# Optimization experiments

Measured on AMD Instinct MI355X. Metric: run time of the kernel, lower is better.

Reference implementation:

```python
import jax, jax.numpy as jnp
import numpy as np

N, IN, OUT, RANK = 8192, 4096, 4096, 16
SCALING = 2.0

def setup_inputs() -> dict:
    key = jax.random.key(0)
    k1, k2, k3, k4 = jax.random.split(key, 4)
    x = jax.random.normal(k1, (N, IN), dtype=jnp.float32)
    weight = jax.random.normal(k2, (OUT, IN), dtype=jnp.float32) * (1.0 / np.sqrt(IN))
    lora_A = jax.random.normal(k3, (RANK, IN), dtype=jnp.float32) * (1.0 / np.sqrt(IN))
    lora_B = jax.random.normal(k4, (OUT, RANK), dtype=jnp.float32) * 0.01
    return {"x": x, "weight": weight, "lora_A": lora_A, "lora_B": lora_B}

def reference(x, weight, lora_A, lora_B):
    # frozen base linear: F.linear(x, weight) == x @ weight.T  -> [N, OUT]
    base = jnp.einsum('ni,oi->no', x, weight)
    # LoRA branch: dropout(x) (p=0 => identity) @ A.T @ B.T, scaled
    lora = jnp.einsum('ni,ri->nr', x, lora_A)      # [N, RANK]
    lora = jnp.einsum('nr,or->no', lora, lora_B)   # [N, OUT]
    return base + lora * SCALING
```

## Files before the change

kernel.cpp:

```cpp
#include <hip/hip_runtime.h>


#define N_ROWS 8192
#define K_DIM  4096
#define N_COLS 4096
#define RANK   16
#define BK     64
#define NT     (K_DIM / BK)

typedef __bf16 bf16x8 __attribute__((ext_vector_type(8)));
typedef float  f32x4  __attribute__((ext_vector_type(4)));

__device__ __forceinline__ unsigned short f2bf(float f) {
  unsigned int u = __builtin_bit_cast(unsigned int, f);
  u += 0x7FFFu + ((u >> 16) & 1u);
  return (unsigned short)(u >> 16);
}


__global__ __launch_bounds__(256) void conv_x_kernel(const float* __restrict__ x,
                                                     unsigned short* __restrict__ xb) {
  size_t idx = (size_t)blockIdx.x * blockDim.x + threadIdx.x;
  const float4 v = *reinterpret_cast<const float4*>(x + idx * 4);
  ushort4 r;
  r.x = f2bf(v.x); r.y = f2bf(v.y); r.z = f2bf(v.z); r.w = f2bf(v.w);
  *reinterpret_cast<ushort4*>(xb + idx * 4) = r;
}

__global__ __launch_bounds__(256) void make_weff_kernel(const float* __restrict__ w,
                                                        const float* __restrict__ A,
                                                        const float* __restrict__ Bm,
                                                        unsigned short* __restrict__ wb) {
  size_t idx = (size_t)blockIdx.x * blockDim.x + threadIdx.x;
  int o  = (int)(idx >> 10);
  int ic = (int)(idx & 1023) << 2;
  const float4 wv = *reinterpret_cast<const float4*>(w + (size_t)o * K_DIM + ic);
  float a0 = wv.x, a1 = wv.y, a2 = wv.z, a3 = wv.w;
  float br[RANK];
#pragma unroll
  for (int r4 = 0; r4 < RANK / 4; ++r4) {
    const float4 bv = *reinterpret_cast<const float4*>(Bm + (size_t)o * RANK + r4 * 4);
    br[r4 * 4 + 0] = bv.x; br[r4 * 4 + 1] = bv.y;
    br[r4 * 4 + 2] = bv.z; br[r4 * 4 + 3] = bv.w;
  }
#pragma unroll
  for (int r = 0; r < RANK; ++r) {
    const float4 av = *reinterpret_cast<const float4*>(A + (size_t)r * K_DIM + ic);
    float b2 = br[r] * 2.0f;
    a0 += b2 * av.x; a1 += b2 * av.y; a2 += b2 * av.z; a3 += b2 * av.w;
  }
  ushort4 rr;
  rr.x = f2bf(a0); rr.y = f2bf(a1); rr.z = f2bf(a2); rr.w = f2bf(a3);
  *reinterpret_cast<ushort4*>(wb + (size_t)o * K_DIM + ic) = rr;
}


__device__ __forceinline__ void gload_lds16(const void* g, void* l) {
  __builtin_amdgcn_global_load_lds(
      (__attribute__((address_space(1))) void*)g,
      (__attribute__((address_space(3))) void*)l, 16, 0, 0);
}

__global__ __launch_bounds__(512, 2) void gemm_bf16_8phase(
    const unsigned short* __restrict__ xb, const unsigned short* __restrict__ wb,
    float* __restrict__ out) {
  __shared__ __align__(16) char smem[131072];

  const int t  = threadIdx.x;
  const int l  = t & 63;
  const int wv = t >> 6;
  const int lr = l & 15;
  const int lk = l >> 4;
  const int wr = wv >> 2;
  const int wc = wv & 3;

  const int bid  = blockIdx.x;
  const int sbid = (bid & 7) * 64 + (bid >> 3);
  const int bm   = sbid >> 4;
  const int bn   = sbid & 15;

  const int srow = t >> 3;
  const int scol = ((t & 7) ^ ((t >> 3) & 7)) << 3;
  const unsigned short* gA = xb + (size_t)(bm * 256 + srow) * K_DIM + scol;
  const unsigned short* gB = wb + (size_t)(bn * 256 + srow) * K_DIM + scol;
  char* ldsA = smem + t * 16;
  char* ldsB = smem + 65536 + t * 16;

#define STAGE_A(hh, tk, bufb) do {                                              \
    const unsigned short* _g = gA + (size_t)((hh) * 128) * K_DIM + (size_t)(tk) * BK; \
    char* _l = ldsA + (bufb) * 32768 + (hh) * 16384;                            \
    gload_lds16(_g, _l);                                                        \
    gload_lds16(_g + (size_t)64 * K_DIM, _l + 8192);                            \
  } while (0)
#define STAGE_B(hh, tk, bufb) do {                                              \
    const unsigned short* _g = gB + (size_t)((hh) * 128) * K_DIM + (size_t)(tk) * BK; \
    char* _l = ldsB + (bufb) * 32768 + (hh) * 16384;                            \
    gload_lds16(_g, _l);                                                        \
    gload_lds16(_g + (size_t)64 * K_DIM, _l + 8192);                            \
  } while (0)

  const int g0   = (lk ^ (lr & 7)) << 4;
  const int g1   = ((lk + 4) ^ (lr & 7)) << 4;
  const int aoff = (wr * 16 + lr) * 128;
  const int boff = (wc * 16 + lr) * 128;

  bf16x8 aF[8];
  bf16x8 bF[4];
  f32x4 acc[8][4];
#pragma unroll
  for (int m = 0; m < 8; ++m)
#pragma unroll
    for (int n = 0; n < 4; ++n)
      acc[m][n] = (f32x4){0.f, 0.f, 0.f, 0.f};

#define READ_A(hh, bufo) do {                                                   \
    const char* _b = smem + (bufo) + (hh) * 16384 + aoff;                       \
    aF[0] = *(const bf16x8*)(_b + 0 * 4096 + g0);                               \
    aF[1] = *(const bf16x8*)(_b + 0 * 4096 + g1);                               \
    aF[2] = *(const bf16x8*)(_b + 1 * 4096 + g0);                               \
    aF[3] = *(const bf16x8*)(_b + 1 * 4096 + g1);                               \
    aF[4] = *(const bf16x8*)(_b + 2 * 4096 + g0);                               \
    aF[5] = *(const bf16x8*)(_b + 2 * 4096 + g1);                               \
    aF[6] = *(const bf16x8*)(_b + 3 * 4096 + g0);                               \
    aF[7] = *(const bf16x8*)(_b + 3 * 4096 + g1);                               \
  } while (0)
#define READ_B(hh, bufo) do {                                                   \
    const char* _b = smem + 65536 + (bufo) + (hh) * 16384 + boff;               \
    bF[0] = *(const bf16x8*)(_b + 0 * 8192 + g0);                               \
    bF[1] = *(const bf16x8*)(_b + 0 * 8192 + g1);                               \
    bF[2] = *(const bf16x8*)(_b + 1 * 8192 + g0);                               \
    bF[3] = *(const bf16x8*)(_b + 1 * 8192 + g1);                               \
  } while (0)

#define MFMA_Q(MB, NB) do {                                                     \
    _Pragma("unroll")                                                           \
    for (int mi = 0; mi < 4; ++mi)                                              \
      _Pragma("unroll")                                                         \
      for (int ni = 0; ni < 2; ++ni)                                            \
        _Pragma("unroll")                                                       \
        for (int kk = 0; kk < 2; ++kk)                                          \
          acc[(MB) + mi][(NB) + ni] = __builtin_amdgcn_mfma_f32_16x16x32_bf16(  \
              aF[mi * 2 + kk], bF[ni * 2 + kk], acc[(MB) + mi][(NB) + ni], 0, 0, 0); \
  } while (0)

#define PH_PRE() do {                                                           \
    __builtin_amdgcn_s_barrier();                                               \
    asm volatile("s_waitcnt lgkmcnt(0)" ::: "memory");                          \
    __builtin_amdgcn_sched_barrier(0);                                          \
    __builtin_amdgcn_s_setprio(1);                                              \
  } while (0)
#define PH_POST() do {                                                          \
    __builtin_amdgcn_s_setprio(0);                                              \
    __builtin_amdgcn_sched_barrier(0);                                          \
    __builtin_amdgcn_s_barrier();                                               \
  } while (0)

  STAGE_A(0, 0, 0); STAGE_A(1, 0, 0); STAGE_B(0, 0, 0); STAGE_B(1, 0, 0);
  STAGE_A(0, 1, 1); STAGE_B(1, 1, 1);
  asm volatile("s_waitcnt vmcnt(4)" ::: "memory");
  __builtin_amdgcn_s_barrier();

  for (int tt = 0; tt < NT; ++tt) {
    const int cbuf = tt & 1;
    const int bufo = cbuf * 32768;
    const int nbuf = cbuf ^ 1;

    READ_A(0, bufo); READ_B(0, bufo);
    if (tt + 1 < NT) STAGE_A(1, tt + 1, nbuf);
    PH_PRE(); MFMA_Q(0, 0); PH_POST();

    READ_B(1, bufo);
    if (tt + 1 < NT) STAGE_B(0, tt + 1, nbuf);
    PH_PRE(); MFMA_Q(0, 2); PH_POST();

    READ_A(1, bufo);
    if (tt + 2 < NT) STAGE_A(0, tt + 2, cbuf);
    PH_PRE(); MFMA_Q(4, 2); PH_POST();

    READ_B(0, bufo);
    if (tt + 2 < NT) STAGE_B(1, tt + 2, cbuf);
    __builtin_amdgcn_s_barrier();
    asm volatile("s_waitcnt lgkmcnt(0)" ::: "memory");
    __builtin_amdgcn_sched_barrier(0);
    __builtin_amdgcn_s_setprio(1);
    MFMA_Q(4, 0);
    __builtin_amdgcn_s_setprio(0);
    __builtin_amdgcn_sched_barrier(0);
    if (tt + 2 < NT) { asm volatile("s_waitcnt vmcnt(4)" ::: "memory"); }
    else             { asm volatile("s_waitcnt vmcnt(0)" ::: "memory"); }
    __builtin_amdgcn_s_barrier();
  }

  const int orow = bm * 256 + wr * 16 + lk * 4;
  const int ocol = bn * 256 + wc * 16 + lr;
#pragma unroll
  for (int mf = 0; mf < 8; ++mf)
#pragma unroll
    for (int nf = 0; nf < 4; ++nf)
#pragma unroll
      for (int j = 0; j < 4; ++j)
        out[(size_t)(orow + mf * 32 + j) * N_COLS + (ocol + nf * 64)] = acc[mf][nf][j];

#undef STAGE_A
#undef STAGE_B
#undef READ_A
#undef READ_B
#undef MFMA_Q
#undef PH_PRE
#undef PH_POST
}


__global__ __launch_bounds__(256) void fallback_kernel(const float* __restrict__ x,
                                                       const float* __restrict__ w,
                                                       const float* __restrict__ A,
                                                       const float* __restrict__ Bm,
                                                       float* __restrict__ out) {
  const int o    = blockIdx.x * 256 + threadIdx.x;
  const int nrow = blockIdx.y;
  float bro[RANK];
#pragma unroll
  for (int r = 0; r < RANK; ++r) bro[r] = Bm[(size_t)o * RANK + r] * 2.0f;
  float bacc = 0.f;
  float tacc[RANK];
#pragma unroll
  for (int r = 0; r < RANK; ++r) tacc[r] = 0.f;
  for (int k = 0; k < K_DIM; ++k) {
    float xv = x[(size_t)nrow * K_DIM + k];
    bacc += xv * w[(size_t)o * K_DIM + k];
#pragma unroll
    for (int r = 0; r < RANK; ++r) tacc[r] += xv * A[(size_t)r * K_DIM + k];
  }
  float res = bacc;
#pragma unroll
  for (int r = 0; r < RANK; ++r) res += bro[r] * tacc[r];
  out[(size_t)nrow * N_COLS + o] = res;
}


extern "C" void kernel_launch(void* const* d_in, const int* in_sizes, int n_in,
                              void* d_out, int out_size, void* d_ws, size_t ws_size,
                              hipStream_t stream) {
  const float* x  = (const float*)d_in[0];
  const float* w  = (const float*)d_in[1];
  const float* A  = (const float*)d_in[2];
  const float* Bm = (const float*)d_in[3];
  float* out = (float*)d_out;

  const size_t need = ((size_t)N_ROWS * K_DIM + (size_t)N_COLS * K_DIM) * sizeof(unsigned short);
  if (ws_size < need) {
    dim3 grid(N_COLS / 256, N_ROWS);
    fallback_kernel<<<grid, 256, 0, stream>>>(x, w, A, Bm, out);
    return;
  }

  unsigned short* xb = (unsigned short*)d_ws;
  unsigned short* wb = xb + (size_t)N_ROWS * K_DIM;

  conv_x_kernel<<<(N_ROWS * K_DIM / 4) / 256, 256, 0, stream>>>(x, xb);
  make_weff_kernel<<<(N_COLS * K_DIM / 4) / 256, 256, 0, stream>>>(w, A, Bm, wb);

  const int grid_gemm = (N_ROWS / 256) * (N_COLS / 256);
  gemm_bf16_8phase<<<grid_gemm, 512, 0, stream>>>(xb, wb, out);
}
```

Before: 319.4 us.

## Restructure bf16 GEMM main loop into register double-buffered software pipeline

Rewrites the GEMM K-loop so LDS fragment reads for the next phase and next tile are issued into separate register sets (even/odd A and B fragments) while MFMAs consume the current ones. Barriers no longer wait on lgkmcnt before every phase. The prefetch distance drops to one tile with finer vmcnt waits, and the loop is unrolled by two to alternate buffers. Launch bounds change from 2 to 1 block per CU to free registers for the extra fragment storage, which may lower occupancy and latency hiding.

```diff
diff --git a/kernel.cpp b/kernel.cpp
--- a/kernel.cpp
+++ b/kernel.cpp
@@ -61,7 +61,7 @@
       (__attribute__((address_space(3))) void*)l, 16, 0, 0);
 }
 
-__global__ __launch_bounds__(512, 2) void gemm_bf16_8phase(
+__global__ __launch_bounds__(512, 1) void gemm_bf16_pipe(
     const unsigned short* __restrict__ xb, const unsigned short* __restrict__ wb,
     float* __restrict__ out) {
   __shared__ __align__(16) char smem[131072];
@@ -86,15 +86,15 @@
   char* ldsA = smem + t * 16;
   char* ldsB = smem + 65536 + t * 16;
 
-#define STAGE_A(hh, tk, bufb) do {                                              \
-    const unsigned short* _g = gA + (size_t)((hh) * 128) * K_DIM + (size_t)(tk) * BK; \
-    char* _l = ldsA + (bufb) * 32768 + (hh) * 16384;                            \
+#define STG_A(hh, SRC, NB) do {                                                 \
+    const unsigned short* _g = (SRC) + (size_t)((hh) * 128) * K_DIM;            \
+    char* _l = ldsA + (NB) + (hh) * 16384;                                      \
     gload_lds16(_g, _l);                                                        \
     gload_lds16(_g + (size_t)64 * K_DIM, _l + 8192);                            \
   } while (0)
-#define STAGE_B(hh, tk, bufb) do {                                              \
-    const unsigned short* _g = gB + (size_t)((hh) * 128) * K_DIM + (size_t)(tk) * BK; \
-    char* _l = ldsB + (bufb) * 32768 + (hh) * 16384;                            \
+#define STG_B(hh, SRC, NB) do {                                                 \
+    const unsigned short* _g = (SRC) + (size_t)((hh) * 128) * K_DIM;            \
+    char* _l = ldsB + (NB) + (hh) * 16384;                                      \
     gload_lds16(_g, _l);                                                        \
     gload_lds16(_g + (size_t)64 * K_DIM, _l + 8192);                            \
   } while (0)
@@ -104,8 +104,7 @@
   const int aoff = (wr * 16 + lr) * 128;
   const int boff = (wc * 16 + lr) * 128;
 
-  bf16x8 aF[8];
-  bf16x8 bF[4];
+  bf16x8 aE[8], aO[8], bO[4], bE[2][4];
   f32x4 acc[8][4];
 #pragma unroll
   for (int m = 0; m < 8; ++m)
@@ -113,82 +112,84 @@
     for (int n = 0; n < 4; ++n)
       acc[m][n] = (f32x4){0.f, 0.f, 0.f, 0.f};
 
-#define READ_A(hh, bufo) do {                                                   \
-    const char* _b = smem + (bufo) + (hh) * 16384 + aoff;                       \
-    aF[0] = *(const bf16x8*)(_b + 0 * 4096 + g0);                               \
-    aF[1] = *(const bf16x8*)(_b + 0 * 4096 + g1);                               \
-    aF[2] = *(const bf16x8*)(_b + 1 * 4096 + g0);                               \
-    aF[3] = *(const bf16x8*)(_b + 1 * 4096 + g1);                               \
-    aF[4] = *(const bf16x8*)(_b + 2 * 4096 + g0);                               \
-    aF[5] = *(const bf16x8*)(_b + 2 * 4096 + g1);                               \
-    aF[6] = *(const bf16x8*)(_b + 3 * 4096 + g0);                               \
-    aF[7] = *(const bf16x8*)(_b + 3 * 4096 + g1);                               \
-  } while (0)
-#define READ_B(hh, bufo) do {                                                   \
-    const char* _b = smem + 65536 + (bufo) + (hh) * 16384 + boff;               \
-    bF[0] = *(const bf16x8*)(_b + 0 * 8192 + g0);                               \
-    bF[1] = *(const bf16x8*)(_b + 0 * 8192 + g1);                               \
-    bF[2] = *(const bf16x8*)(_b + 1 * 8192 + g0);                               \
-    bF[3] = *(const bf16x8*)(_b + 1 * 8192 + g1);                               \
-  } while (0)
-
-#define MFMA_Q(MB, NB) do {                                                     \
+#define RD_A(DST, BASE) do {                                                    \
+    _Pragma("unroll")                                                           \
+    for (int m = 0; m < 4; ++m) {                                               \
+      DST[2 * m + 0] = *(const bf16x8*)(smem + (BASE) + m * 4096 + aoff + g0);  \
+      DST[2 * m + 1] = *(const bf16x8*)(smem + (BASE) + m * 4096 + aoff + g1);  \
+    }                                                                           \
+  } while (0)
+#define RD_B(DST, BASE) do {                                                    \
+    _Pragma("unroll")                                                           \
+    for (int n = 0; n < 2; ++n) {                                               \
+      DST[2 * n + 0] = *(const bf16x8*)(smem + 65536 + (BASE) + n * 8192 + boff + g0); \
+      DST[2 * n + 1] = *(const bf16x8*)(smem + 65536 + (BASE) + n * 8192 + boff + g1); \
+    }                                                                           \
+  } while (0)
+
+#define MFMA_Q(MB, AF, NB0, BF) do {                                            \
     _Pragma("unroll")                                                           \
     for (int mi = 0; mi < 4; ++mi)                                              \
       _Pragma("unroll")                                                         \
       for (int ni = 0; ni < 2; ++ni)                                            \
         _Pragma("unroll")                                                       \
         for (int kk = 0; kk < 2; ++kk)                                          \
-          acc[(MB) + mi][(NB) + ni] = __builtin_amdgcn_mfma_f32_16x16x32_bf16(  \
-              aF[mi * 2 + kk], bF[ni * 2 + kk], acc[(MB) + mi][(NB) + ni], 0, 0, 0); \
-  } while (0)
-
-#define PH_PRE() do {                                                           \
+          acc[(MB) + mi][(NB0) + ni] = __builtin_amdgcn_mfma_f32_16x16x32_bf16( \
+              AF[mi * 2 + kk], BF[ni * 2 + kk], acc[(MB) + mi][(NB0) + ni], 0, 0, 0); \
+  } while (0)
+
+#define PH_BAR() do {                                                           \
+    __builtin_amdgcn_sched_barrier(0);                                          \
     __builtin_amdgcn_s_barrier();                                               \
-    asm volatile("s_waitcnt lgkmcnt(0)" ::: "memory");                          \
-    __builtin_amdgcn_sched_barrier(0);                                          \
-    __builtin_amdgcn_s_setprio(1);                                              \
-  } while (0)
-#define PH_POST() do {                                                          \
-    __builtin_amdgcn_s_setprio(0);                                              \
-    __builtin_amdgcn_sched_barrier(0);                                          \
+    __builtin_amdgcn_sched_barrier(0);                                          \
+  } while (0)
+#define PH_BAR_VM(VM) do {                                                      \
+    __builtin_amdgcn_sched_barrier(0);                                          \
+    asm volatile("s_waitcnt vmcnt(" #VM ")" ::: "memory");                      \
     __builtin_amdgcn_s_barrier();                                               \
-  } while (0)
-
-  STAGE_A(0, 0, 0); STAGE_A(1, 0, 0); STAGE_B(0, 0, 0); STAGE_B(1, 0, 0);
-  STAGE_A(0, 1, 1); STAGE_B(1, 1, 1);
-  asm volatile("s_waitcnt vmcnt(4)" ::: "memory");
+    __builtin_amdgcn_sched_barrier(0);                                          \
+  } while (0)
+
+#define TILE(CB, NB, PC, PN, T) do {                                            \
+    const int _tk = ((T) + 1 < NT) ? (T) + 1 : NT - 1;                          \
+    const unsigned short* _sA = gA + (size_t)_tk * BK;                          \
+    const unsigned short* _sB = gB + (size_t)_tk * BK;                          \
+                                                                       \
+    RD_B(bO, (CB) + 16384);                                                     \
+    STG_A(0, _sA, NB); STG_A(1, _sA, NB);                                       \
+    __builtin_amdgcn_s_setprio(1); MFMA_Q(0, aE, 0, bE[PC]);                    \
+    __builtin_amdgcn_s_setprio(0);                                              \
+    PH_BAR();                                                                   \
+                                                                       \
+    RD_A(aO, (CB) + 16384);                                                     \
+    STG_B(0, _sB, NB); STG_B(1, _sB, NB);                                       \
+    __builtin_amdgcn_s_setprio(1); MFMA_Q(0, aE, 2, bO);                        \
+    __builtin_amdgcn_s_setprio(0);                                              \
+    PH_BAR_VM(4);                                                               \
+                                                                       \
+    RD_A(aE, (NB));                                                             \
+    __builtin_amdgcn_s_setprio(1); MFMA_Q(4, aO, 2, bO);                        \
+    __builtin_amdgcn_s_setprio(0);                                              \
+    PH_BAR_VM(2);                                                               \
+                                                                       \
+    RD_B(bE[PN], (NB));                                                         \
+    __builtin_amdgcn_s_setprio(1); MFMA_Q(4, aO, 0, bE[PC]);                    \
+    __builtin_amdgcn_s_setprio(0);                                              \
+    PH_BAR_VM(0);                                                               \
+  } while (0)
+
+  STG_A(0, gA, 0); STG_A(1, gA, 0); STG_B(0, gB, 0); STG_B(1, gB, 0);
+  __builtin_amdgcn_sched_barrier(0);
+  asm volatile("s_waitcnt vmcnt(0)" ::: "memory");
   __builtin_amdgcn_s_barrier();
-
-  for (int tt = 0; tt < NT; ++tt) {
-    const int cbuf = tt & 1;
-    const int bufo = cbuf * 32768;
-    const int nbuf = cbuf ^ 1;
-
-    READ_A(0, bufo); READ_B(0, bufo);
-    if (tt + 1 < NT) STAGE_A(1, tt + 1, nbuf);
-    PH_PRE(); MFMA_Q(0, 0); PH_POST();
-
-    READ_B(1, bufo);
-    if (tt + 1 < NT) STAGE_B(0, tt + 1, nbuf);
-    PH_PRE(); MFMA_Q(0, 2); PH_POST();
-
-    READ_A(1, bufo);
-    if (tt + 2 < NT) STAGE_A(0, tt + 2, cbuf);
-    PH_PRE(); MFMA_Q(4, 2); PH_POST();
-
-    READ_B(0, bufo);
-    if (tt + 2 < NT) STAGE_B(1, tt + 2, cbuf);
-    __builtin_amdgcn_s_barrier();
-    asm volatile("s_waitcnt lgkmcnt(0)" ::: "memory");
-    __builtin_amdgcn_sched_barrier(0);
-    __builtin_amdgcn_s_setprio(1);
-    MFMA_Q(4, 0);
-    __builtin_amdgcn_s_setprio(0);
-    __builtin_amdgcn_sched_barrier(0);
-    if (tt + 2 < NT) { asm volatile("s_waitcnt vmcnt(4)" ::: "memory"); }
-    else             { asm volatile("s_waitcnt vmcnt(0)" ::: "memory"); }
-    __builtin_amdgcn_s_barrier();
+  __builtin_amdgcn_sched_barrier(0);
+  RD_A(aE, 0);
+  RD_B(bE[0], 0);
+
+#pragma nounroll
+  for (int u = 0; u < NT / 2; ++u) {
+    TILE(0, 32768, 0, 1, 2 * u);
+    TILE(32768, 0, 1, 0, 2 * u + 1);
   }
 
   const int orow = bm * 256 + wr * 16 + lk * 4;
@@ -201,13 +202,14 @@
       for (int j = 0; j < 4; ++j)
         out[(size_t)(orow + mf * 32 + j) * N_COLS + (ocol + nf * 64)] = acc[mf][nf][j];
 
-#undef STAGE_A
-#undef STAGE_B
-#undef READ_A
-#undef READ_B
+#undef STG_A
+#undef STG_B
+#undef RD_A
+#undef RD_B
 #undef MFMA_Q
-#undef PH_PRE
-#undef PH_POST
+#undef PH_BAR
+#undef PH_BAR_VM
+#undef TILE
 }
 
 
@@ -261,5 +263,5 @@
   make_weff_kernel<<<(N_COLS * K_DIM / 4) / 256, 256, 0, stream>>>(w, A, Bm, wb);
 
   const int grid_gemm = (N_ROWS / 256) * (N_COLS / 256);
-  gemm_bf16_8phase<<<grid_gemm, 512, 0, stream>>>(xb, wb, out);
-}
+  gemm_bf16_pipe<<<grid_gemm, 512, 0, stream>>>(xb, wb, out);
+}
```

Measured after the change: 333.3 us. +4.3%, slower.
